# Performance work log

Hardware: AMD Instinct MI355X
Metric: run time of the kernel (lower is better)

Reference implementation:

```python
import jax, jax.numpy as jnp
import numpy as np


def _box_filter(img):
    # img: [B,1,H,W]; 5x5 uniform kernel, padding=4 -> output [B,1,H+4,W+4]
    k = jnp.full((1, 1, 5, 5), 1.0 / 25.0, dtype=img.dtype)
    return jax.lax.conv_general_dilated(
        img, k, window_strides=(1, 1), padding=((4, 4), (4, 4)),
        dimension_numbers=('NCHW', 'OIHW', 'NCHW'))


def setup_inputs() -> dict:
    key = jax.random.key(0)
    k1, k2 = jax.random.split(key)
    x = jax.random.normal(k1, (64, 1, 512, 512), dtype=jnp.float32)
    y = jax.random.normal(k2, (64, 1, 512, 512), dtype=jnp.float32)
    return {"x": x, "y": y}


def reference(x, y):
    diff = _box_filter(x) - _box_filter(y)
    # faithful to torch.mean(torch.sqrt(diff * diff)) (== mean(|diff|))
    return jnp.mean(jnp.sqrt(diff * diff))
```

## Files before the change

### kernel.cpp

```cpp
#include <hip/hip_runtime.h>


#define IMG_W 512
#define IMG_H 512
#define OUT_W 516
#define OUT_H 516
#define TR    16
#define NT    256

__global__ __launch_bounds__(NT) void box_loss_kernel(
    const float* __restrict__ x, const float* __restrict__ y,
    float* __restrict__ partial)
{
    __shared__ float ring[5][IMG_W];
    __shared__ float vbuf[2][OUT_W + 4];
    __shared__ float wsum[NT / 64];

    const int t  = threadIdx.x;
    const int b  = blockIdx.y;
    const int i0 = blockIdx.x * TR;
    const int c0 = 2 * t;

    const float* xb = x + (size_t)b * IMG_W * IMG_H;
    const float* yb = y + (size_t)b * IMG_W * IMG_H;

    #pragma unroll
    for (int s = 0; s < 5; ++s) {
        ring[s][c0] = 0.f; ring[s][c0 + 1] = 0.f;
    }
    if (t < 4) {
        vbuf[0][t] = 0.f;         vbuf[1][t] = 0.f;
        vbuf[0][OUT_W + t] = 0.f; vbuf[1][OUT_W + t] = 0.f;
    }

    float v0 = 0.f, v1 = 0.f;
    for (int r = i0 - 4; r < i0; ++r) {
        float d0 = 0.f, d1 = 0.f;
        if (r >= 0) {
            float2 xv = *(const float2*)(xb + (size_t)r * IMG_W + c0);
            float2 yv = *(const float2*)(yb + (size_t)r * IMG_W + c0);
            d0 = xv.x - yv.x; d1 = xv.y - yv.y;
        }
        int slot = (r + 5) % 5;
        ring[slot][c0] = d0; ring[slot][c0 + 1] = d1;
        v0 += d0; v1 += d1;
    }

    const int nrows = min(TR, OUT_H - i0);
    float acc = 0.f;
    int buf = 0;
    for (int ii = 0; ii < nrows; ++ii) {
        const int i = i0 + ii;
        float d0 = 0.f, d1 = 0.f;
        if (i < IMG_H) {
            float2 xv = *(const float2*)(xb + (size_t)i * IMG_W + c0);
            float2 yv = *(const float2*)(yb + (size_t)i * IMG_W + c0);
            d0 = xv.x - yv.x; d1 = xv.y - yv.y;
        }
        const int slot = i % 5;
        float o0 = ring[slot][c0], o1 = ring[slot][c0 + 1];
        v0 += d0 - o0; v1 += d1 - o1;
        ring[slot][c0] = d0; ring[slot][c0 + 1] = d1;

        vbuf[buf][4 + c0]     = v0;
        vbuf[buf][4 + c0 + 1] = v1;
        __syncthreads();

        const float* __restrict__ vb = vbuf[buf];
        float s0 = vb[t]     + vb[t + 1]   + vb[t + 2]   + vb[t + 3]   + vb[t + 4];
        float s1 = vb[t+256] + vb[t + 257] + vb[t + 258] + vb[t + 259] + vb[t + 260];
        acc += fabsf(s0) + fabsf(s1);
        if (t < 4) {
            float s2 = vb[t+512] + vb[t+513] + vb[t+514] + vb[t+515] + vb[t+516];
            acc += fabsf(s2);
        }
        buf ^= 1;
    }

    #pragma unroll
    for (int off = 32; off > 0; off >>= 1)
        acc += __shfl_down(acc, off, 64);
    if ((t & 63) == 0) wsum[t >> 6] = acc;
    __syncthreads();
    if (t == 0) {
        float s = wsum[0] + wsum[1] + wsum[2] + wsum[3];
        atomicAdd(partial, s);
    }
}

__global__ void finalize_kernel(const float* __restrict__ partial,
                                float* __restrict__ out)
{
    out[0] = partial[0] * (1.0f / (25.0f * 64.0f * 516.0f * 516.0f));
}

extern "C" void kernel_launch(void* const* d_in, const int* in_sizes, int n_in,
                              void* d_out, int out_size, void* d_ws, size_t ws_size,
                              hipStream_t stream) {
    const float* x = (const float*)d_in[0];
    const float* y = (const float*)d_in[1];
    float* out = (float*)d_out;
    float* ws  = (float*)d_ws;

    hipMemsetAsync(ws, 0, sizeof(float), stream);

    dim3 grid((OUT_H + TR - 1) / TR, 64);
    box_loss_kernel<<<grid, NT, 0, stream>>>(x, y, ws);
    finalize_kernel<<<1, 1, 0, stream>>>(ws, out);
}
```

Baseline: 170.0 us.

## Rewrite box loss as per-wave strips with register sliding window and shuffles

Each wavefront now processes a 12-row strip of one image, with each lane holding 8 contiguous columns in registers. The vertical 5-row window is kept in a register ring, and the horizontal 5-tap sum uses shuffles between neighbouring lanes instead of shared-memory buffers and per-row __syncthreads. The separate finalize kernel is folded into the main kernel through a last-block atomic counter. This removes block-wide barriers and LDS traffic and drops one launch. In exchange, more halo rows are reloaded because strips are shorter, and register pressure rises.

After: 172.4 us. Within noise of the previous version (+1.5%).

```diff
diff --git a/kernel.cpp b/kernel.cpp
--- a/kernel.cpp
+++ b/kernel.cpp
@@ -1,97 +1,105 @@
 #include <hip/hip_runtime.h>
 
 
-#define IMG_W 512
-#define IMG_H 512
-#define OUT_W 516
-#define OUT_H 516
-#define TR    16
-#define NT    256
+#define TR      12
+#define STRIPS  43
+#define NWAVES  (64 * STRIPS)
+#define NBLOCKS (NWAVES / 4)
 
-__global__ __launch_bounds__(NT) void box_loss_kernel(
+__global__ __launch_bounds__(256) void box_loss_kernel(
     const float* __restrict__ x, const float* __restrict__ y,
-    float* __restrict__ partial)
+    float* __restrict__ ws, float* __restrict__ out)
 {
-    __shared__ float ring[5][IMG_W];
-    __shared__ float vbuf[2][OUT_W + 4];
-    __shared__ float wsum[NT / 64];
+    __shared__ float wsum[4];
 
-    const int t  = threadIdx.x;
-    const int b  = blockIdx.y;
-    const int i0 = blockIdx.x * TR;
-    const int c0 = 2 * t;
+    const int lane  = threadIdx.x & 63;
+    const int wid   = (blockIdx.x << 2) + (threadIdx.x >> 6);
+    const int img   = wid / STRIPS;
+    const int strip = wid - img * STRIPS;
+    const int i0    = strip * TR;
 
-    const float* xb = x + (size_t)b * IMG_W * IMG_H;
-    const float* yb = y + (size_t)b * IMG_W * IMG_H;
+    const size_t base = (size_t)img * (512 * 512) + (size_t)(lane * 8);
+    const float* xb = x + base;
+    const float* yb = y + base;
+
+    float hist[5][8];
+    float v[8];
+    #pragma unroll
+    for (int j = 0; j < 8; ++j) v[j] = 0.f;
+    #pragma unroll
+    for (int s = 0; s < 5; ++s)
+        #pragma unroll
+        for (int j = 0; j < 8; ++j) hist[s][j] = 0.f;
+
+    float acc = 0.f;
 
     #pragma unroll
-    for (int s = 0; s < 5; ++s) {
-        ring[s][c0] = 0.f; ring[s][c0 + 1] = 0.f;
-    }
-    if (t < 4) {
-        vbuf[0][t] = 0.f;         vbuf[1][t] = 0.f;
-        vbuf[0][OUT_W + t] = 0.f; vbuf[1][OUT_W + t] = 0.f;
-    }
+    for (int k = 0; k < TR + 4; ++k) {
+        const int r  = i0 - 4 + k;
+        const int rc = min(max(r, 0), 511);
+        const bool valid = (r == rc);
+        const float* xr = xb + (size_t)rc * 512;
+        const float* yr = yb + (size_t)rc * 512;
+        float4 xa = ((const float4*)xr)[0];
+        float4 xc = ((const float4*)xr)[1];
+        float4 ya = ((const float4*)yr)[0];
+        float4 yc = ((const float4*)yr)[1];
 
-    float v0 = 0.f, v1 = 0.f;
-    for (int r = i0 - 4; r < i0; ++r) {
-        float d0 = 0.f, d1 = 0.f;
-        if (r >= 0) {
-            float2 xv = *(const float2*)(xb + (size_t)r * IMG_W + c0);
-            float2 yv = *(const float2*)(yb + (size_t)r * IMG_W + c0);
-            d0 = xv.x - yv.x; d1 = xv.y - yv.y;
+        float d[8];
+        d[0] = xa.x - ya.x; d[1] = xa.y - ya.y; d[2] = xa.z - ya.z; d[3] = xa.w - ya.w;
+        d[4] = xc.x - yc.x; d[5] = xc.y - yc.y; d[6] = xc.z - yc.z; d[7] = xc.w - yc.w;
+        #pragma unroll
+        for (int j = 0; j < 8; ++j) d[j] = valid ? d[j] : 0.f;
+
+        const int slot = k % 5;
+        #pragma unroll
+        for (int j = 0; j < 8; ++j) {
+            v[j] += d[j] - hist[slot][j];
+            hist[slot][j] = d[j];
         }
-        int slot = (r + 5) % 5;
-        ring[slot][c0] = d0; ring[slot][c0 + 1] = d1;
-        v0 += d0; v1 += d1;
-    }
 
-    const int nrows = min(TR, OUT_H - i0);
-    float acc = 0.f;
-    int buf = 0;
-    for (int ii = 0; ii < nrows; ++ii) {
-        const int i = i0 + ii;
-        float d0 = 0.f, d1 = 0.f;
-        if (i < IMG_H) {
-            float2 xv = *(const float2*)(xb + (size_t)i * IMG_W + c0);
-            float2 yv = *(const float2*)(yb + (size_t)i * IMG_W + c0);
-            d0 = xv.x - yv.x; d1 = xv.y - yv.y;
+        if (k >= 4) {
+            float h0 = __shfl_up(v[4], 1, 64);
+            float h1 = __shfl_up(v[5], 1, 64);
+            float h2 = __shfl_up(v[6], 1, 64);
+            float h3 = __shfl_up(v[7], 1, 64);
+            if (lane == 0) { h0 = 0.f; h1 = 0.f; h2 = 0.f; h3 = 0.f; }
+
+            float s = h0 + h1 + h2 + h3 + v[0];
+            acc += fabsf(s);
+            s += v[1] - h0;  acc += fabsf(s);
+            s += v[2] - h1;  acc += fabsf(s);
+            s += v[3] - h2;  acc += fabsf(s);
+            s += v[4] - h3;  acc += fabsf(s);
+            s += v[5] - v[0]; acc += fabsf(s);
+            s += v[6] - v[1]; acc += fabsf(s);
+            s += v[7] - v[2]; acc += fabsf(s);
+            if (lane == 63) {
+                float t = v[7];  acc += fabsf(t);
+                t += v[6];       acc += fabsf(t);
+                t += v[5];       acc += fabsf(t);
+                t += v[4];       acc += fabsf(t);
+            }
         }
-        const int slot = i % 5;
-        float o0 = ring[slot][c0], o1 = ring[slot][c0 + 1];
-        v0 += d0 - o0; v1 += d1 - o1;
-        ring[slot][c0] = d0; ring[slot][c0 + 1] = d1;
-
-        vbuf[buf][4 + c0]     = v0;
-        vbuf[buf][4 + c0 + 1] = v1;
-        __syncthreads();
-
-        const float* __restrict__ vb = vbuf[buf];
-        float s0 = vb[t]     + vb[t + 1]   + vb[t + 2]   + vb[t + 3]   + vb[t + 4];
-        float s1 = vb[t+256] + vb[t + 257] + vb[t + 258] + vb[t + 259] + vb[t + 260];
-        acc += fabsf(s0) + fabsf(s1);
-        if (t < 4) {
-            float s2 = vb[t+512] + vb[t+513] + vb[t+514] + vb[t+515] + vb[t+516];
-            acc += fabsf(s2);
-        }
-        buf ^= 1;
     }
 
     #pragma unroll
     for (int off = 32; off > 0; off >>= 1)
         acc += __shfl_down(acc, off, 64);
-    if ((t & 63) == 0) wsum[t >> 6] = acc;
+    if (lane == 0) wsum[threadIdx.x >> 6] = acc;
     __syncthreads();
-    if (t == 0) {
+
+    if (threadIdx.x == 0) {
         float s = wsum[0] + wsum[1] + wsum[2] + wsum[3];
-        atomicAdd(partial, s);
+        atomicAdd(ws, s);
+        __threadfence();
+        unsigned* cnt = (unsigned*)(ws + 1);
+        unsigned done = atomicAdd(cnt, 1u);
+        if (done == (unsigned)(gridDim.x - 1)) {
+            float total = atomicAdd(ws, 0.0f);
+            out[0] = total * (1.0f / (25.0f * 64.0f * 516.0f * 516.0f));
+        }
     }
-}
-
-__global__ void finalize_kernel(const float* __restrict__ partial,
-                                float* __restrict__ out)
-{
-    out[0] = partial[0] * (1.0f / (25.0f * 64.0f * 516.0f * 516.0f));
 }
 
 extern "C" void kernel_launch(void* const* d_in, const int* in_sizes, int n_in,
@@ -102,9 +110,7 @@
     float* out = (float*)d_out;
     float* ws  = (float*)d_ws;
 
-    hipMemsetAsync(ws, 0, sizeof(float), stream);
+    hipMemsetAsync(ws, 0, 8, stream);
 
-    dim3 grid((OUT_H + TR - 1) / TR, 64);
-    box_loss_kernel<<<grid, NT, 0, stream>>>(x, y, ws);
-    finalize_kernel<<<1, 1, 0, stream>>>(ws, out);
+    box_loss_kernel<<<NBLOCKS, 256, 0, stream>>>(x, y, ws, out);
 }
```
